# Optimization experiments

Measured on AMD Instinct MI355X. Metric: run time of the kernel, lower is better.

The kernel has to match this reference:

```python
import jax, jax.numpy as jnp
import numpy as np
from jax import lax

B, N, D = 32, 256, 128  # graphs, nodes-per-graph, embed_dim
T = B * N               # total nodes


def _mlp(x, W1, b1, W2, b2):
    # Linear -> ReLU -> Linear (query_proj / key_proj)
    return jnp.maximum(x @ W1.T + b1, 0.0) @ W2.T + b2


def _l2norm(x):
    # F.normalize(dim=-1), eps=1e-12
    return x / jnp.maximum(jnp.linalg.norm(x, axis=-1, keepdims=True), 1e-12)


def _gru_cell(x, h, W_ih, W_hh, b_ih, b_hh):
    # torch.nn.GRU single-step cell, gate order (r, z, n)
    gi = x @ W_ih.T + b_ih
    gh = h @ W_hh.T + b_hh
    ir, iz, inn = jnp.split(gi, 3, axis=-1)
    hr, hz, hn = jnp.split(gh, 3, axis=-1)
    r = jax.nn.sigmoid(ir + hr)
    z = jax.nn.sigmoid(iz + hz)
    n = jnp.tanh(inn + r * hn)
    return (1.0 - z) * n + z * h


def setup_inputs() -> dict:
    key = jax.random.key(0)
    ks = jax.random.split(key, 16)
    s = float(1.0 / np.sqrt(D))
    u = lambda k, sh: jax.random.uniform(k, sh, jnp.float32, -s, s)
    return {
        "node_embeddings": jax.random.normal(ks[0], (T, D), jnp.float32),
        "start_nodes": jnp.arange(B, dtype=jnp.int32) * N,  # first node of each graph
        "batch_idx": jnp.repeat(jnp.arange(B, dtype=jnp.int32), N),
        "Wq1": u(ks[1], (D, D)), "bq1": u(ks[2], (D,)),
        "Wq2": u(ks[3], (D, D)), "bq2": u(ks[4], (D,)),
        "Wk1": u(ks[5], (D, D)), "bk1": u(ks[6], (D,)),
        "Wk2": u(ks[7], (D, D)), "bk2": u(ks[8], (D,)),
        "W_ih": u(ks[9], (3 * D, D)), "W_hh": u(ks[10], (3 * D, D)),
        "b_ih": u(ks[11], (3 * D,)), "b_hh": u(ks[12], (3 * D,)),
        "v": jax.random.normal(ks[13], (D,), jnp.float32),
        "Wh": u(ks[14], (D, D)), "bh": u(ks[15], (D,)),
    }


def reference(node_embeddings, start_nodes, batch_idx, Wq1, bq1, Wq2, bq2,
              Wk1, bk1, Wk2, bk2, W_ih, W_hh, b_ih, b_hh, v, Wh, bh):
    Bn = start_nodes.shape[0]
    Tn = node_embeddings.shape[0]
    steps = Tn // Bn - 1  # equal-size graphs: N-1 decode steps after start node

    # graph contexts = per-graph mean of node embeddings -> hidden init
    ones = jnp.ones((Tn,), jnp.float32)
    counts = jax.ops.segment_sum(ones, batch_idx, num_segments=Bn)
    gctx = jax.ops.segment_sum(node_embeddings, batch_idx, num_segments=Bn) / counts[:, None]
    hidden0 = gctx @ Wh.T + bh                       # [B, D]

    # keys are recomputed identically every step in torch; hoist (same math)
    keys = _l2norm(_mlp(node_embeddings, Wk1, bk1, Wk2, bk2))  # [T, D]
    member = batch_idx[None, :] == jnp.arange(Bn)[:, None]     # [B, T]

    def step(carry, _):
        hidden, current, mask = carry
        mask = mask.at[current].set(False)           # visit current nodes
        x = node_embeddings[current]                 # [B, D]
        h = _gru_cell(x, hidden, W_ih, W_hh, b_ih, b_hh)
        q = _l2norm(_mlp(h, Wq1, bq1, Wq2, bq2))     # [B, D]
        # scores over ALL nodes, then masked to own-graph unvisited (as in torch)
        scores = jnp.einsum('btd,d->bt', jnp.tanh(keys[None] + q[:, None, :]), v)
        valid = member & mask[None, :]
        scores = jnp.where(valid, scores, -jnp.inf)
        probs = jax.nn.softmax(scores, axis=1)
        logp = jnp.log(probs + 1e-10)
        nxt = jnp.argmax(probs, axis=1).astype(current.dtype)  # eval-mode greedy
        lp = jnp.take_along_axis(logp, nxt[:, None], axis=1)[:, 0]
        return (h, nxt, mask), (current, lp)

    init = (hidden0, start_nodes, jnp.ones((Tn,), bool))
    (_, cur, _), (tour_steps, lps) = lax.scan(jax.checkpoint(step), init, None, length=steps)
    tours = jnp.concatenate([tour_steps, cur[None]], axis=0).T  # [B, N]
    log_probs = lps.T                                           # [B, N-1]
    return tours, log_probs
```

## Files before the change

kernel.cpp:

```cpp
#include <hip/hip_runtime.h>
#include <hip/hip_bf16.h>
#include <math.h>

#define DD   128
#define NPG  256
#define NGR  32
#define TTOT 8192
#define LOG2E  1.4426950408889634f
#define LOG2E2 2.8853900817779268f
#define KSTRIDE 264
#define SSTR    268
#define H2A(j)  ((j) + (((j)>>5)<<3))
#define PAD16(j) ((j) + (((j)>>4)<<2))

__device__ __forceinline__ float dot4(float4 a, float4 b){
  return a.x*b.x + a.y*b.y + a.z*b.z + a.w*b.w;
}
template<int CTRL, int RMASK>
__device__ __forceinline__ float upd_f(float oldv, float x){
  return __int_as_float(__builtin_amdgcn_update_dpp(
      __float_as_int(oldv), __float_as_int(x), CTRL, RMASK, 0xf, false));
}
__device__ __forceinline__ float dpp_xor1(float x){
  return __int_as_float(__builtin_amdgcn_mov_dpp(__float_as_int(x), 0xB1, 0xf, 0xf, false));
}
__device__ __forceinline__ float dpp_xor2(float x){
  return __int_as_float(__builtin_amdgcn_mov_dpp(__float_as_int(x), 0x4E, 0xf, 0xf, false));
}
__device__ __forceinline__ float quad_sum_dpp(float x){
  float s = x + dpp_xor1(x);
  return s + dpp_xor2(s);
}
__device__ __forceinline__ float dpp_wave_sum(float x){
  x += upd_f<0x111,0xf>(0.f, x);
  x += upd_f<0x112,0xf>(0.f, x);
  x += upd_f<0x114,0xf>(0.f, x);
  x += upd_f<0x118,0xf>(0.f, x);
  x += upd_f<0x142,0xa>(0.f, x);
  x += upd_f<0x143,0xc>(0.f, x);
  return __uint_as_float(__builtin_amdgcn_readlane(__float_as_uint(x), 63));
}
__device__ __forceinline__ float dpp_wave_max(float x){
  const float NI = -INFINITY;
  x = fmaxf(x, upd_f<0x111,0xf>(NI, x));
  x = fmaxf(x, upd_f<0x112,0xf>(NI, x));
  x = fmaxf(x, upd_f<0x114,0xf>(NI, x));
  x = fmaxf(x, upd_f<0x118,0xf>(NI, x));
  x = fmaxf(x, upd_f<0x142,0xa>(NI, x));
  x = fmaxf(x, upd_f<0x143,0xc>(NI, x));
  return __uint_as_float(__builtin_amdgcn_readlane(__float_as_uint(x), 63));
}
__device__ __forceinline__ float sigfast(float x){
  return __builtin_amdgcn_rcpf(1.f + __builtin_amdgcn_exp2f(-x*LOG2E));
}
__device__ __forceinline__ float tanhfast(float y){
  return 1.f - 2.f*__builtin_amdgcn_rcpf(1.f + __builtin_amdgcn_exp2f(y*LOG2E2));
}


__device__ __forceinline__ void load_w128(float* Ws, const float* __restrict__ W, int t){
  const float4* src = (const float4*)W;
  #pragma unroll
  for (int m=0;m<16;m++){
    int idx = m*256+t; int r = idx>>5, c4 = idx&31;
    float4 val = src[idx];
    float* dst = &Ws[r*129 + c4*4];
    dst[0]=val.x; dst[1]=val.y; dst[2]=val.z; dst[3]=val.w;
  }
}

__device__ __forceinline__ void mm_tile(const float* __restrict__ inS, const float* __restrict__ Ws,
                                        float acc[4][4], int jg, int ng){
  #pragma unroll
  for(int r=0;r<4;r++)
    #pragma unroll
    for(int c=0;c<4;c++) acc[r][c]=0.f;
  #pragma unroll 4
  for (int k=0;k<128;k++){
    float w[4], x[4];
    #pragma unroll
    for (int r=0;r<4;r++) w[r] = Ws[(jg*4+r)*129+k];
    #pragma unroll
    for (int c=0;c<4;c++) x[c] = inS[(ng*4+c)*129+k];
    #pragma unroll
    for (int r=0;r<4;r++)
      #pragma unroll
      for (int c=0;c<4;c++) acc[r][c] += w[r]*x[c];
  }
}

__global__ __launch_bounds__(256) void precompute_kernel(
    const float* __restrict__ emb,
    const float* __restrict__ Wk1, const float* __restrict__ bk1,
    const float* __restrict__ Wk2, const float* __restrict__ bk2,
    const float* __restrict__ Wih, const float* __restrict__ bih,
    float* __restrict__ keysE, float* __restrict__ giall)
{
  __shared__ __align__(16) float xs[32*129];
  __shared__ __align__(16) float Ws[128*129];
  __shared__ __align__(16) float hs[32*129];
  __shared__ __align__(16) float os[32*129];
  __shared__ float nrm[32];
  const int t  = threadIdx.x;
  const int n0 = blockIdx.x * 32;
  const int ng = t & 7, jg = t >> 3;

  {
    const float4* src = (const float4*)emb + (size_t)n0*32;
    #pragma unroll
    for (int m=0;m<4;m++){
      int idx = m*256+t; int n = idx>>5, c4 = idx&31;
      float4 val = src[idx];
      float* dst = &xs[n*129 + c4*4];
      dst[0]=val.x; dst[1]=val.y; dst[2]=val.z; dst[3]=val.w;
    }
  }
  load_w128(Ws, Wk1, t);
  __syncthreads();
  {
    float acc[4][4];
    mm_tile(xs, Ws, acc, jg, ng);
    #pragma unroll
    for (int r=0;r<4;r++){
      float bb = bk1[jg*4+r];
      #pragma unroll
      for (int c=0;c<4;c++) hs[(ng*4+c)*129 + jg*4+r] = fmaxf(acc[r][c]+bb, 0.f);
    }
  }
  __syncthreads();
  load_w128(Ws, Wk2, t);
  __syncthreads();
  {
    float acc[4][4];
    mm_tile(hs, Ws, acc, jg, ng);
    #pragma unroll
    for (int r=0;r<4;r++){
      float bb = bk2[jg*4+r];
      #pragma unroll
      for (int c=0;c<4;c++) os[(ng*4+c)*129 + jg*4+r] = acc[r][c]+bb;
    }
  }
  __syncthreads();
  if (t<32){
    float ss=0.f;
    for (int j=0;j<128;j++){ float x = os[t*129+j]; ss += x*x; }
    nrm[t] = fmaxf(sqrtf(ss), 1e-12f);
  }
  __syncthreads();
  #pragma unroll
  for (int m=0;m<16;m++){
    int idx = m*256+t; int nl = idx & 31, d = idx >> 5;
    float kk = os[nl*129 + d] / nrm[nl];
    keysE[(size_t)d*TTOT + n0 + nl] = __builtin_amdgcn_exp2f(kk * LOG2E2);
  }
  for (int c=0;c<3;c++){
    __syncthreads();
    load_w128(Ws, Wih + c*16384, t);
    __syncthreads();
    float acc[4][4];
    mm_tile(xs, Ws, acc, jg, ng);
    #pragma unroll
    for (int r=0;r<4;r++){
      float bb = bih[c*128 + jg*4+r];
      #pragma unroll
      for (int cc=0;cc<4;cc++)
        giall[(size_t)(n0 + ng*4+cc)*384 + c*128 + jg*4 + r] = acc[r][cc] + bb;
    }
  }
}


__global__ __launch_bounds__(512, 2) void decode_kernel(
    const float* __restrict__ emb,
    const float* __restrict__ keysE, const float* __restrict__ giall,
    const float* __restrict__ Whh, const float* __restrict__ bhh,
    const float* __restrict__ Wq1, const float* __restrict__ bq1,
    const float* __restrict__ Wq2, const float* __restrict__ bq2,
    const float* __restrict__ v,   const float* __restrict__ Wh,
    const float* __restrict__ bh,  const int* __restrict__ start_nodes,
    float* __restrict__ tours_o, float* __restrict__ lp_o)
{
  __shared__ __align__(16) float keys_s[128*KSTRIDE];
  __shared__ __align__(16) float h_s[2][160];
  __shared__ __align__(16) float qh_s[160];
  __shared__ __align__(16) float q_s[128];
  __shared__ __align__(16) float eq_s[160];
  __shared__ __align__(16) float v_sp[160];
  __shared__ __align__(16) float spartS[8*SSTR];
  __shared__ int col2node_s[256], node2col_s[256];
  __shared__ float redv[8]; __shared__ int redi[8]; __shared__ float red2[8];

  const int t = threadIdx.x;
  const int b = blockIdx.x;
  const int g  = t >> 2, s3 = t & 3;
  const int w  = t >> 6, L  = t & 63;
  const int oct = L & 7, dgrp = L >> 3;

  float4 whh4[3][8], wq14[8], wq24[8];
  {
    const float4* w0  = (const float4*)(Whh + (size_t)(g      )*128 + s3*32);
    const float4* w1  = (const float4*)(Whh + (size_t)(128 + g)*128 + s3*32);
    const float4* w2  = (const float4*)(Whh + (size_t)(256 + g)*128 + s3*32);
    const float4* q1p = (const float4*)(Wq1 + (size_t)g*128 + s3*32);
    const float4* q2p = (const float4*)(Wq2 + (size_t)g*128 + s3*32);
    #pragma unroll
    for (int i=0;i<8;i++){
      whh4[0][i]=w0[i]; whh4[1][i]=w1[i]; whh4[2][i]=w2[i];
      wq14[i]=q1p[i];   wq24[i]=q2p[i];
    }
  }
  const float br = bhh[g], bz = bhh[128+g], bn = bhh[256+g];
  const float b1g = bq1[g], b2g = bq2[g];

  if (t<128) v_sp[PAD16(t)] = -2.f * v[t];
  if (t<256){ col2node_s[t] = t; node2col_s[t] = t; }
  {
    #pragma unroll
    for (int m=0;m<16;m++){
      int idx = m*512 + t; int d = idx>>6, q = idx&63;
      *(float4*)(keys_s + d*KSTRIDE + q*4) =
        *(const float4*)(keysE + (size_t)d*TTOT + b*256 + q*4);
    }
  }
  {
    int d = t & 127, part = t >> 7;
    float a = 0.f;
    const float* base = emb + (size_t)(b*256 + part*64)*128 + d;
    for (int i=0;i<64;i++) a += base[(size_t)i*128];
    spartS[part*128+d] = a;
  }
  int cur = start_nodes[b];
  __syncthreads();
  if (t<128){
    float a = 0.f;
    #pragma unroll
    for (int p=0;p<4;p++) a += spartS[p*128+t];
    q_s[t] = a * (1.f/256.f);
  }
  __syncthreads();
  if (t<128){
    float a = bh[t];
    const float* wr = Wh + (size_t)t*128;
    for (int k=0;k<128;k++) a += wr[k]*q_s[k];
    h_s[0][H2A(t)] = a;
  }
  {
    float xv = (t<128) ? v[t] : 0.f;
    float tot = dpp_wave_sum(xv);
    if (L==0) red2[w] = tot;
  }
  __syncthreads();
  float sv = 0.f;
  #pragma unroll
  for (int i=0;i<8;i++) sv += red2[i];

  float gir=0.f, giz=0.f, gin=0.f;
  if (s3==0){
    const float* gp = giall + (size_t)cur*384 + g;
    gir = gp[0]; giz = gp[128]; gin = gp[256];
  }

  for (int step=0; step<255; step++){
    const int par = step & 1;
    const int V   = 255 - step;
    const int curl = cur - b*256;

    if (t < 128){
      int px = node2col_s[curl];
      keys_s[t*KSTRIDE + px] = keys_s[t*KSTRIDE + V];
    }
    if (t == 0) tours_o[b*256+step] = (float)cur;

    {
      float a0=0.f,a1=0.f,a2=0.f;
      const float4* hc4 = (const float4*)(h_s[par] + s3*40);
      #pragma unroll
      for (int i=0;i<8;i++){
        float4 hv = hc4[i];
        a0 += dot4(whh4[0][i], hv);
        a1 += dot4(whh4[1][i], hv);
        a2 += dot4(whh4[2][i], hv);
      }
      a0 = quad_sum_dpp(a0);
      a1 = quad_sum_dpp(a1);
      a2 = quad_sum_dpp(a2);
      if (s3==0){
        float r = sigfast(gir + a0 + br);
        float z = sigfast(giz + a1 + bz);
        float n = tanhfast(gin + r*(a2 + bn));
        h_s[par^1][H2A(g)] = (1.f-z)*n + z*h_s[par][H2A(g)];
      }
    }
    __syncthreads();

    if (t == 0){
      int px = node2col_s[curl];
      int ln = col2node_s[V];
      col2node_s[px] = ln;
      node2col_s[ln] = px;
    }

    {
      float a=0.f;
      const float4* hc4 = (const float4*)(h_s[par^1] + s3*40);
      #pragma unroll
      for (int i=0;i<8;i++) a += dot4(wq14[i], hc4[i]);
      a = quad_sum_dpp(a);
      if (s3==0) qh_s[H2A(g)] = fmaxf(a + b1g, 0.f);
    }
    __syncthreads();

    {
      float a=0.f;
      const float4* qc4 = (const float4*)(qh_s + s3*40);
      #pragma unroll
      for (int i=0;i<8;i++) a += dot4(wq24[i], qc4[i]);
      a = quad_sum_dpp(a);
      float qval = a + b2g;
      if (s3==0) q_s[g] = qval;
      float ssp = (s3==0) ? qval*qval : 0.f;
      float tot = dpp_wave_sum(ssp);
      if (L==0) red2[w] = tot;
    }
    __syncthreads();

    if (t<128){
      float ss = 0.f;
      #pragma unroll
      for (int i=0;i<8;i++) ss += red2[i];
      float rn = 1.f / fmaxf(sqrtf(ss), 1e-12f);
      eq_s[PAD16(t)] = __builtin_amdgcn_exp2f(q_s[t] * rn * LOG2E2);
    }
    __syncthreads();

    if (32*w < V){
      const float* kbase = keys_s + dgrp*16*KSTRIDE + 32*w + oct*4;
      const float* ebase = eq_s  + dgrp*20;
      const float* vbase = v_sp  + dgrp*20;
      float4 acc = {0.f,0.f,0.f,0.f};
      #pragma unroll
      for (int jj=0;jj<16;jj++){
        float eqj = ebase[jj];
        float vj  = vbase[jj];
        float4 K = *(const float4*)(kbase + jj*KSTRIDE);
        float r0 = __builtin_amdgcn_rcpf(fmaf(K.x, eqj, 1.f));
        float r1 = __builtin_amdgcn_rcpf(fmaf(K.y, eqj, 1.f));
        float r2 = __builtin_amdgcn_rcpf(fmaf(K.z, eqj, 1.f));
        float r3 = __builtin_amdgcn_rcpf(fmaf(K.w, eqj, 1.f));
        acc.x = fmaf(vj, r0, acc.x);
        acc.y = fmaf(vj, r1, acc.y);
        acc.z = fmaf(vj, r2, acc.z);
        acc.w = fmaf(vj, r3, acc.w);
      }
      *(float4*)(spartS + dgrp*SSTR + 32*w + oct*4) = acc;
    }
    __syncthreads();

    if (t < 256){
      float val;
      if (t < V){
        float sum = 0.f;
        #pragma unroll
        for (int i=0;i<8;i++) sum += spartS[i*SSTR + t];
        val = sv + sum;
      } else val = -INFINITY;
      float m = dpp_wave_max(val);
      unsigned long long mk = __ballot(val == m);
      int ri = (w<<6) + (__ffsll(mk) - 1);
      float e = (t < V) ? __builtin_amdgcn_exp2f((val - m)*LOG2E) : 0.f;
      float Sw = dpp_wave_sum(e);
      if (L==0){ redv[w]=m; redi[w]=ri; red2[w]=Sw; }
    }
    __syncthreads();

    {
      float m = redv[0]; int besti = redi[0];
      #pragma unroll
      for (int i=1;i<4;i++){
        float ov=redv[i]; int oi=redi[i];
        if (ov > m || (ov==m && oi<besti)){ m=ov; besti=oi; }
      }
      cur = b*256 + col2node_s[besti];
      if (s3==0){
        const float* gp = giall + (size_t)cur*384 + g;
        gir = gp[0]; giz = gp[128]; gin = gp[256];
      }
      if (t==0){
        float sum = 0.f;
        #pragma unroll
        for (int i=0;i<4;i++)
          sum += red2[i] * __builtin_amdgcn_exp2f((redv[i]-m)*LOG2E);
        lp_o[b*255+step] = logf(1.f/sum + 1e-10f);
      }
    }
  }
  if (t==0) tours_o[b*256+255] = (float)cur;
}

extern "C" void kernel_launch(void* const* d_in, const int* in_sizes, int n_in,
                              void* d_out, int out_size, void* d_ws, size_t ws_size,
                              hipStream_t stream) {
  const float* emb  = (const float*)d_in[0];
  const int*   startn = (const int*)d_in[1];
  const float* Wq1 = (const float*)d_in[3];  const float* bq1 = (const float*)d_in[4];
  const float* Wq2 = (const float*)d_in[5];  const float* bq2 = (const float*)d_in[6];
  const float* Wk1 = (const float*)d_in[7];  const float* bk1 = (const float*)d_in[8];
  const float* Wk2 = (const float*)d_in[9];  const float* bk2 = (const float*)d_in[10];
  const float* Wih = (const float*)d_in[11]; const float* Whh = (const float*)d_in[12];
  const float* bih = (const float*)d_in[13]; const float* bhh = (const float*)d_in[14];
  const float* v   = (const float*)d_in[15]; const float* Wh  = (const float*)d_in[16];
  const float* bh  = (const float*)d_in[17];

  float* keysE = (float*)d_ws;
  float* giall = keysE + (size_t)TTOT*DD;

  float* outp = (float*)d_out;

  precompute_kernel<<<256, 256, 0, stream>>>(emb, Wk1, bk1, Wk2, bk2, Wih, bih, keysE, giall);
  decode_kernel<<<NGR, 512, 0, stream>>>(emb, keysE, giall, Whh, bhh, Wq1, bq1, Wq2, bq2,
                                         v, Wh, bh, startn, outp, outp + TTOT);
}
```

Baseline: 893.7 us.

## Remove two per-step barriers by recomputing exp(q) and redundant per-wave argmax

The separate exp(2q·rn) pass into eq_s, with its barrier, is removed. Each thread now computes the exponential inline inside the score loop from the padded q_s. The final score reduction and argmax/softmax sum are done redundantly by every wave, each handling 4 columns per lane, which removes the cross-wave redv/redi barrier and reduction. Small serial tasks (key swap, tour write, col/node map update, lp write) move to threads in other waves so they can overlap with wave 0. In exchange the exp work is duplicated across threads and every wave repeats the 256-wide reduction.

```diff
diff --git a/kernel.cpp b/kernel.cpp
--- a/kernel.cpp
+++ b/kernel.cpp
@@ -183,12 +183,11 @@
   __shared__ __align__(16) float keys_s[128*KSTRIDE];
   __shared__ __align__(16) float h_s[2][160];
   __shared__ __align__(16) float qh_s[160];
-  __shared__ __align__(16) float q_s[128];
-  __shared__ __align__(16) float eq_s[160];
+  __shared__ __align__(16) float q_s[160];
   __shared__ __align__(16) float v_sp[160];
   __shared__ __align__(16) float spartS[8*SSTR];
   __shared__ int col2node_s[256], node2col_s[256];
-  __shared__ float redv[8]; __shared__ int redi[8]; __shared__ float red2[8];
+  __shared__ float red2[8];
 
   const int t = threadIdx.x;
   const int b = blockIdx.x;
@@ -265,11 +264,12 @@
     const int V   = 255 - step;
     const int curl = cur - b*256;
 
-    if (t < 128){
+    if (t >= 128 && t < 256){
+      int r = t - 128;
       int px = node2col_s[curl];
-      keys_s[t*KSTRIDE + px] = keys_s[t*KSTRIDE + V];
-    }
-    if (t == 0) tours_o[b*256+step] = (float)cur;
+      keys_s[r*KSTRIDE + px] = keys_s[r*KSTRIDE + V];
+    }
+    if (t == 384) tours_o[b*256+step] = (float)cur;
 
     {
       float a0=0.f,a1=0.f,a2=0.f;
@@ -293,7 +293,7 @@
     }
     __syncthreads();
 
-    if (t == 0){
+    if (t == 448){
       int px = node2col_s[curl];
       int ln = col2node_s[V];
       col2node_s[px] = ln;
@@ -317,30 +317,25 @@
       for (int i=0;i<8;i++) a += dot4(wq24[i], qc4[i]);
       a = quad_sum_dpp(a);
       float qval = a + b2g;
-      if (s3==0) q_s[g] = qval;
+      if (s3==0) q_s[PAD16(g)] = qval;
       float ssp = (s3==0) ? qval*qval : 0.f;
       float tot = dpp_wave_sum(ssp);
       if (L==0) red2[w] = tot;
     }
     __syncthreads();
 
-    if (t<128){
+    if (32*w < V){
       float ss = 0.f;
       #pragma unroll
       for (int i=0;i<8;i++) ss += red2[i];
       float rn = 1.f / fmaxf(sqrtf(ss), 1e-12f);
-      eq_s[PAD16(t)] = __builtin_amdgcn_exp2f(q_s[t] * rn * LOG2E2);
-    }
-    __syncthreads();
-
-    if (32*w < V){
       const float* kbase = keys_s + dgrp*16*KSTRIDE + 32*w + oct*4;
-      const float* ebase = eq_s  + dgrp*20;
-      const float* vbase = v_sp  + dgrp*20;
+      const float* qb    = q_s  + dgrp*20;
+      const float* vbase = v_sp + dgrp*20;
       float4 acc = {0.f,0.f,0.f,0.f};
       #pragma unroll
       for (int jj=0;jj<16;jj++){
-        float eqj = ebase[jj];
+        float eqj = __builtin_amdgcn_exp2f(qb[jj] * rn * LOG2E2);
         float vj  = vbase[jj];
         float4 K = *(const float4*)(kbase + jj*KSTRIDE);
         float r0 = __builtin_amdgcn_rcpf(fmaf(K.x, eqj, 1.f));
@@ -356,45 +351,41 @@
     }
     __syncthreads();
 
-    if (t < 256){
-      float val;
-      if (t < V){
-        float sum = 0.f;
-        #pragma unroll
-        for (int i=0;i<8;i++) sum += spartS[i*SSTR + t];
-        val = sv + sum;
-      } else val = -INFINITY;
-      float m = dpp_wave_max(val);
-      unsigned long long mk = __ballot(val == m);
-      int ri = (w<<6) + (__ffsll(mk) - 1);
-      float e = (t < V) ? __builtin_amdgcn_exp2f((val - m)*LOG2E) : 0.f;
-      float Sw = dpp_wave_sum(e);
-      if (L==0){ redv[w]=m; redi[w]=ri; red2[w]=Sw; }
-    }
-    __syncthreads();
-
     {
-      float m = redv[0]; int besti = redi[0];
-      #pragma unroll
-      for (int i=1;i<4;i++){
-        float ov=redv[i]; int oi=redi[i];
-        if (ov > m || (ov==m && oi<besti)){ m=ov; besti=oi; }
+      const float* sp = spartS + 4*L;
+      float sx=0.f, sy=0.f, sz=0.f, sw=0.f;
+      #pragma unroll
+      for (int i=0;i<8;i++){
+        float4 p = *(const float4*)(sp + i*SSTR);
+        sx += p.x; sy += p.y; sz += p.z; sw += p.w;
       }
+      int c0 = 4*L;
+      float vx = (c0+0 < V) ? sv+sx : -INFINITY;
+      float vy = (c0+1 < V) ? sv+sy : -INFINITY;
+      float vz = (c0+2 < V) ? sv+sz : -INFINITY;
+      float vw = (c0+3 < V) ? sv+sw : -INFINITY;
+      float bm = vx; int bc = c0;
+      if (vy > bm){ bm=vy; bc=c0+1; }
+      if (vz > bm){ bm=vz; bc=c0+2; }
+      if (vw > bm){ bm=vw; bc=c0+3; }
+      float m = dpp_wave_max(bm);
+      unsigned long long mk = __ballot(bm == m);
+      int flane = __ffsll(mk) - 1;
+      int besti = __builtin_amdgcn_readlane(bc, flane);
+      float es = __builtin_amdgcn_exp2f((vx-m)*LOG2E) + __builtin_amdgcn_exp2f((vy-m)*LOG2E)
+               + __builtin_amdgcn_exp2f((vz-m)*LOG2E) + __builtin_amdgcn_exp2f((vw-m)*LOG2E);
+      float S = dpp_wave_sum(es);
       cur = b*256 + col2node_s[besti];
       if (s3==0){
         const float* gp = giall + (size_t)cur*384 + g;
         gir = gp[0]; giz = gp[128]; gin = gp[256];
       }
-      if (t==0){
-        float sum = 0.f;
-        #pragma unroll
-        for (int i=0;i<4;i++)
-          sum += red2[i] * __builtin_amdgcn_exp2f((redv[i]-m)*LOG2E);
-        lp_o[b*255+step] = logf(1.f/sum + 1e-10f);
-      }
+      if (t==320) lp_o[b*255+step] = logf(1.f/S + 1e-10f);
     }
   }
   if (t==0) tours_o[b*256+255] = (float)cur;
+
+  (void)oct;
 }
 
 extern "C" void kernel_launch(void* const* d_in, const int* in_sizes, int n_in,
```

Result: no change. 886.4 us (-0.8%).
